# Kernel optimization log

Hardware: AMD Instinct MI355X
Metric: run time of the kernel (lower is better)

Reference implementation:

```python
import jax, jax.numpy as jnp
import numpy as np

D = 512  # c_size == q_size


def setup_inputs() -> dict:
    key = jax.random.key(0)
    ks = jax.random.split(key, 8)
    c = jax.random.normal(ks[0], (8, 2048, D), dtype=jnp.float32)
    q = jax.random.normal(ks[1], (8, 512, D), dtype=jnp.float32)
    sc = 1.0 / np.sqrt(D)
    w_c = jax.random.uniform(ks[2], (D,), jnp.float32, -sc, sc)
    b_c = jax.random.uniform(ks[3], (), jnp.float32, -sc, sc)
    w_q = jax.random.uniform(ks[4], (D,), jnp.float32, -sc, sc)
    b_q = jax.random.uniform(ks[5], (), jnp.float32, -sc, sc)
    w_cq = jax.random.uniform(ks[6], (D,), jnp.float32, -sc, sc)
    b_cq = jax.random.uniform(ks[7], (), jnp.float32, -sc, sc)
    return {"c": c, "q": q, "w_c": w_c, "b_c": b_c, "w_q": w_q, "b_q": b_q,
            "w_cq": w_cq, "b_cq": b_cq}


def reference(c, q, w_c, b_c, w_q, b_q, w_cq, b_cq):
    # s[b,t,i] = <c[b,t],w_c>+b_c + <q[b,i],w_q>+b_q + <c[b,t]*q[b,i], w_cq>+b_cq
    # The original per-query-token loop for att_weight_cq(c*qi) collapses to
    # a single batched contraction since the Linear is linear in c*qi.
    sc = jnp.einsum('btd,d->bt', c, w_c) + b_c          # (B, c_len)
    sq = jnp.einsum('bid,d->bi', q, w_q) + b_q          # (B, q_len)
    scq = jnp.einsum('btd,bid->bti', c * w_cq, q) + b_cq  # (B, c_len, q_len)
    s = sc[:, :, None] + sq[:, None, :] + scq

    a = jax.nn.softmax(s, axis=2)                       # attend over q
    c2q = jnp.einsum('bti,bid->btd', a, q)              # (B, c_len, D)

    b = jax.nn.softmax(jnp.max(s, axis=2), axis=1)      # (B, c_len)
    q2c = jnp.einsum('bt,btd->bd', b, c)                # (B, D)
    q2c = jnp.broadcast_to(q2c[:, None, :], c.shape)    # (B, c_len, D)

    x = jnp.concatenate([c, c2q, c * c2q, c * q2c], axis=-1)
    return x
```

## Files before the change

kernel.cpp:

```cpp
#include <hip/hip_runtime.h>
#include <cstdint>


constexpr int kB = 8;
constexpr int kT = 2048;
constexpr int kI = 512;
constexpr int kD = 512;
constexpr int kW = 4 * kD;
constexpr int kRows = 64;
constexpr int kTiles = kT / kRows;
constexpr int kChunk = kRows * 72;

using f32x4  = __attribute__((ext_vector_type(4))) float;
using bf16x4 = __attribute__((ext_vector_type(4))) __bf16;
using bf16x8 = __attribute__((ext_vector_type(8))) __bf16;

__device__ __forceinline__ float dot8(const f32x4& a0, const f32x4& a1,
                                      const f32x4& b0, const f32x4& b1) {
  return a0.x * b0.x + a0.y * b0.y + a0.z * b0.z + a0.w * b0.w +
         a1.x * b1.x + a1.y * b1.y + a1.z * b1.z + a1.w * b1.w;
}

__global__ __launch_bounds__(256) void prep_kernel(
    const float* __restrict__ q, const float* __restrict__ w_q,
    const float* __restrict__ b_q, float* __restrict__ sq,
    __bf16* __restrict__ qf, __bf16* __restrict__ vf) {
  const int b = blockIdx.y;
  const int tid = threadIdx.x;
  if (blockIdx.x < 32) {
    __shared__ float sacc[16][17];
    const int g = blockIdx.x;
    const int kk0 = tid >> 6;
    const int lane = tid & 63;
    const int lr = lane & 15, lg = lane >> 4;
    const float* row = q + ((size_t)(b * kI + g * 16 + lr)) * kD;
    float sp = 0.f;
#pragma unroll
    for (int kk = kk0; kk < 16; kk += 4) {
      const int ka = kk * 32 + lg * 8;
      f32x4 v0 = *(const f32x4*)(row + ka);
      f32x4 v1 = *(const f32x4*)(row + ka + 4);
      f32x4 u0 = *(const f32x4*)(w_q + ka);
      f32x4 u1 = *(const f32x4*)(w_q + ka + 4);
      sp += dot8(v0, v1, u0, u1);
      bf16x8 o = {(__bf16)v0.x, (__bf16)v0.y, (__bf16)v0.z, (__bf16)v0.w,
                  (__bf16)v1.x, (__bf16)v1.y, (__bf16)v1.z, (__bf16)v1.w};
      *(bf16x8*)(qf + ((((size_t)(b * 32 + g)) * 16 + kk) << 9) + lane * 8) = o;
    }
    sacc[lr][kk0 * 4 + lg] = sp;
    __syncthreads();
    if (tid < 16) {
      float s = 0.f;
#pragma unroll
      for (int j = 0; j < 16; ++j) s += sacc[tid][j];
      sq[b * kI + g * 16 + tid] = s + b_q[0];
    }
  } else {
    __shared__ float ts[64][68];
    const int blk = blockIdx.x - 32;
    const int i0 = (blk & 7) * 64;
    const int d0 = (blk >> 3) * 64;
    const int r = tid >> 2;
    const int cg = (tid & 3) * 16;
#pragma unroll
    for (int j = 0; j < 4; ++j) {
      f32x4 v = *(const f32x4*)(q + ((size_t)(b * kI + i0 + r)) * kD + d0 + cg + 4 * j);
      ts[r][cg + 4 * j + 0] = v.x;
      ts[r][cg + 4 * j + 1] = v.y;
      ts[r][cg + 4 * j + 2] = v.z;
      ts[r][cg + 4 * j + 3] = v.w;
    }
    __syncthreads();
    const int dl = tid >> 2;
    const int ig = (tid & 3) * 16;
    bf16x8 o0, o1;
#pragma unroll
    for (int j = 0; j < 8; ++j) o0[j] = (__bf16)ts[ig + j][dl];
#pragma unroll
    for (int j = 0; j < 8; ++j) o1[j] = (__bf16)ts[ig + 8 + j][dl];
    const int gd = (d0 >> 4) + (dl >> 4);
    const int lr = dl & 15;
    const int kki0 = (i0 >> 5) + (ig >> 5);
    const int lg0 = (ig & 31) >> 3;
    const int i1 = ig + 8;
    const int kki1 = (i0 >> 5) + (i1 >> 5);
    const int lg1 = (i1 & 31) >> 3;
    *(bf16x8*)(vf + ((((size_t)(b * 32 + gd)) * 16 + kki0) << 9) +
               (lg0 * 16 + lr) * 8) = o0;
    *(bf16x8*)(vf + ((((size_t)(b * 32 + gd)) * 16 + kki1) << 9) +
               (lg1 * 16 + lr) * 8) = o1;
  }
}

__global__ __launch_bounds__(512, 1) void fused_attn(
    const float* __restrict__ c, const __bf16* __restrict__ qf,
    const __bf16* __restrict__ vf, const float* __restrict__ w_cq,
    const float* __restrict__ w_c, const float* __restrict__ b_c,
    const float* __restrict__ b_cq, const float* __restrict__ sq,
    float* __restrict__ out, float* __restrict__ mz,
    float* __restrict__ u_tile) {
  __shared__ __align__(16) char lAP[16 * kChunk];
  __shared__ float scrow[kRows];
  __shared__ float redm[8 * kRows];
  __shared__ float reds[8 * kRows];

  const int b = blockIdx.y;
  const int tile = blockIdx.x;
  const int t0 = tile * kRows;
  const int tid = threadIdx.x;
  const int w = tid >> 6;
  const int lane = tid & 63;
  const int lr = lane & 15, lg = lane >> 4;

  const __bf16* qfb = qf + (((size_t)(b * 32 + w * 4)) * 16 << 9) + lane * 8;
  bf16x8 b0[4], b1[4], b2[4], b3[4];
#pragma unroll
  for (int n4 = 0; n4 < 4; ++n4)
    b0[n4] = *(const bf16x8*)(qfb + (((size_t)(n4 * 16 + 0)) << 9));
#pragma unroll
  for (int n4 = 0; n4 < 4; ++n4)
    b1[n4] = *(const bf16x8*)(qfb + (((size_t)(n4 * 16 + 1)) << 9));
#pragma unroll
  for (int n4 = 0; n4 < 4; ++n4)
    b2[n4] = *(const bf16x8*)(qfb + (((size_t)(n4 * 16 + 2)) << 9));

  {
    const int srow = tid >> 3;
    const int col4 = (tid & 7) * 4;
    const float* crow = c + ((size_t)(b * kT + t0 + srow)) * kD;
    float* orow0 = out + ((size_t)(b * kT + t0 + srow)) * kW;
    float scp = 0.f;
#pragma unroll
    for (int j = 0; j < 16; ++j) {
      const int col = col4 + j * 32;
      f32x4 v = *(const f32x4*)(crow + col);
      *(f32x4*)(orow0 + col) = v;
      const f32x4 wq = *(const f32x4*)(w_cq + col);
      const f32x4 wc = *(const f32x4*)(w_c + col);
      scp += v.x * wc.x + v.y * wc.y + v.z * wc.z + v.w * wc.w;
      v *= wq;
      bf16x4 bv = {(__bf16)v.x, (__bf16)v.y, (__bf16)v.z, (__bf16)v.w};
      *(bf16x4*)(lAP + j * kChunk + srow * 72 + col4 * 2) = bv;
    }
    scp += __shfl_xor(scp, 1, 64);
    scp += __shfl_xor(scp, 2, 64);
    scp += __shfl_xor(scp, 4, 64);
    if ((tid & 7) == 0) scrow[srow] = scp + b_c[0];
  }
  __syncthreads();

  f32x4 acc[4][4] = {};
  bf16x8 afc[4], afn[4];
#pragma unroll
  for (int m = 0; m < 4; ++m)
    afc[m] = *(const bf16x8*)(lAP + 0 * kChunk + (m * 16 + lr) * 72 + lg * 16);
#pragma unroll
  for (int kk = 0; kk < 16; ++kk) {
    if (kk < 13) {
#pragma unroll
      for (int n4 = 0; n4 < 4; ++n4)
        b3[n4] = *(const bf16x8*)(qfb + (((size_t)(n4 * 16 + kk + 3)) << 9));
    }
    if (kk < 15) {
#pragma unroll
      for (int m = 0; m < 4; ++m)
        afn[m] = *(const bf16x8*)(lAP + (kk + 1) * kChunk + (m * 16 + lr) * 72 +
                                  lg * 16);
    }
#pragma unroll
    for (int m = 0; m < 4; ++m)
#pragma unroll
      for (int n4 = 0; n4 < 4; ++n4)
        acc[m][n4] = __builtin_amdgcn_mfma_f32_16x16x32_bf16(afc[m], b0[n4],
                                                             acc[m][n4], 0, 0, 0);
#pragma unroll
    for (int m = 0; m < 4; ++m) afc[m] = afn[m];
#pragma unroll
    for (int n4 = 0; n4 < 4; ++n4) {
      b0[n4] = b1[n4];
      b1[n4] = b2[n4];
      b2[n4] = b3[n4];
    }
  }

  const float bq = b_cq[0];
  float sqv[4];
#pragma unroll
  for (int n4 = 0; n4 < 4; ++n4) sqv[n4] = sq[b * kI + w * 64 + n4 * 16 + lr];
  float scr[4][4];
#pragma unroll
  for (int m = 0; m < 4; ++m)
#pragma unroll
    for (int r = 0; r < 4; ++r) scr[m][r] = scrow[m * 16 + lg * 4 + r] + bq;
#pragma unroll
  for (int m = 0; m < 4; ++m)
#pragma unroll
    for (int n4 = 0; n4 < 4; ++n4)
#pragma unroll
      for (int r = 0; r < 4; ++r) acc[m][n4][r] += scr[m][r] + sqv[n4];

  float mx[4][4];
#pragma unroll
  for (int m = 0; m < 4; ++m)
#pragma unroll
    for (int r = 0; r < 4; ++r) {
      float v = acc[m][0][r];
#pragma unroll
      for (int n4 = 1; n4 < 4; ++n4) v = fmaxf(v, acc[m][n4][r]);
#pragma unroll
      for (int off = 1; off <= 8; off <<= 1) v = fmaxf(v, __shfl_xor(v, off, 64));
      mx[m][r] = v;
    }
  if (lr == 0) {
#pragma unroll
    for (int m = 0; m < 4; ++m)
#pragma unroll
      for (int r = 0; r < 4; ++r)
        redm[w * kRows + m * 16 + lg * 4 + r] = mx[m][r];
  }
  __syncthreads();
#pragma unroll
  for (int m = 0; m < 4; ++m)
#pragma unroll
    for (int r = 0; r < 4; ++r) {
      const int rw = m * 16 + lg * 4 + r;
      float v = redm[rw];
#pragma unroll
      for (int w2 = 1; w2 < 8; ++w2) v = fmaxf(v, redm[w2 * kRows + rw]);
      mx[m][r] = v;
    }

  float sm[4][4] = {};
#pragma unroll
  for (int m = 0; m < 4; ++m)
#pragma unroll
    for (int n4 = 0; n4 < 4; ++n4)
#pragma unroll
      for (int r = 0; r < 4; ++r) {
        const float p = __expf(acc[m][n4][r] - mx[m][r]);
        acc[m][n4][r] = p;
        sm[m][r] += p;
      }
#pragma unroll
  for (int m = 0; m < 4; ++m)
#pragma unroll
    for (int r = 0; r < 4; ++r)
#pragma unroll
      for (int off = 1; off <= 8; off <<= 1)
        sm[m][r] += __shfl_xor(sm[m][r], off, 64);
  if (lr == 0) {
#pragma unroll
    for (int m = 0; m < 4; ++m)
#pragma unroll
      for (int r = 0; r < 4; ++r)
        reds[w * kRows + m * 16 + lg * 4 + r] = sm[m][r];
  }
  __syncthreads();
  float inv[4][4];
#pragma unroll
  for (int m = 0; m < 4; ++m)
#pragma unroll
    for (int r = 0; r < 4; ++r) {
      const int rw = m * 16 + lg * 4 + r;
      float v = reds[rw];
#pragma unroll
      for (int w2 = 1; w2 < 8; ++w2) v += reds[w2 * kRows + rw];
      inv[m][r] = 1.f / v;
    }

  const __bf16* vfb = vf + (((size_t)(b * 32 + w * 4)) * 16 << 9) + lane * 8;
  bf16x8 v0_[4], v1_[4], v2_[4], v3_[4];
#pragma unroll
  for (int n4 = 0; n4 < 4; ++n4)
    v0_[n4] = *(const bf16x8*)(vfb + (((size_t)(n4 * 16 + 0)) << 9));
#pragma unroll
  for (int n4 = 0; n4 < 4; ++n4)
    v1_[n4] = *(const bf16x8*)(vfb + (((size_t)(n4 * 16 + 1)) << 9));
#pragma unroll
  for (int n4 = 0; n4 < 4; ++n4)
    v2_[n4] = *(const bf16x8*)(vfb + (((size_t)(n4 * 16 + 2)) << 9));

#pragma unroll
  for (int m = 0; m < 4; ++m)
#pragma unroll
    for (int r = 0; r < 4; ++r) {
      const int trow = m * 16 + lg * 4 + r;
#pragma unroll
      for (int n4 = 0; n4 < 4; ++n4) {
        const int icol = w * 64 + n4 * 16 + lr;
        const int kkc = icol >> 5, kc = icol & 31;
        *(__bf16*)(lAP + kkc * kChunk + trow * 72 + kc * 2) =
            (__bf16)(acc[m][n4][r] * inv[m][r]);
      }
    }
  __syncthreads();

  float cfrag[4][4][4];
#pragma unroll
  for (int m = 0; m < 4; ++m)
#pragma unroll
    for (int r = 0; r < 4; ++r) {
      const float* crow2 =
          c + ((size_t)(b * kT + t0 + m * 16 + lg * 4 + r)) * kD + w * 64 + lr;
#pragma unroll
      for (int n4 = 0; n4 < 4; ++n4) cfrag[m][n4][r] = crow2[n4 * 16];
    }

  f32x4 o[4][4] = {};
  bf16x8 pfc[4], pfn[4];
#pragma unroll
  for (int m = 0; m < 4; ++m)
    pfc[m] = *(const bf16x8*)(lAP + 0 * kChunk + (m * 16 + lr) * 72 + lg * 16);
#pragma unroll
  for (int kki = 0; kki < 16; ++kki) {
    if (kki < 13) {
#pragma unroll
      for (int n4 = 0; n4 < 4; ++n4)
        v3_[n4] = *(const bf16x8*)(vfb + (((size_t)(n4 * 16 + kki + 3)) << 9));
    }
    if (kki < 15) {
#pragma unroll
      for (int m = 0; m < 4; ++m)
        pfn[m] = *(const bf16x8*)(lAP + (kki + 1) * kChunk + (m * 16 + lr) * 72 +
                                  lg * 16);
    }
#pragma unroll
    for (int m = 0; m < 4; ++m)
#pragma unroll
      for (int n4 = 0; n4 < 4; ++n4)
        o[m][n4] = __builtin_amdgcn_mfma_f32_16x16x32_bf16(pfc[m], v0_[n4],
                                                           o[m][n4], 0, 0, 0);
#pragma unroll
    for (int m = 0; m < 4; ++m) pfc[m] = pfn[m];
#pragma unroll
    for (int n4 = 0; n4 < 4; ++n4) {
      v0_[n4] = v1_[n4];
      v1_[n4] = v2_[n4];
      v2_[n4] = v3_[n4];
    }
  }

  float m_tile;
  {
    float v = mx[0][0];
#pragma unroll
    for (int m = 0; m < 4; ++m)
#pragma unroll
      for (int r = 0; r < 4; ++r) v = fmaxf(v, mx[m][r]);
    v = fmaxf(v, __shfl_xor(v, 16, 64));
    v = fmaxf(v, __shfl_xor(v, 32, 64));
    m_tile = v;
  }
  float u[4] = {};
  float zz = 0.f;
#pragma unroll
  for (int m = 0; m < 4; ++m)
#pragma unroll
    for (int r = 0; r < 4; ++r) {
      const int t = t0 + m * 16 + lg * 4 + r;
      const size_t rb = (size_t)(b * kT + t);
      float* orow = out + rb * kW;
      const float ev = __expf(mx[m][r] - m_tile);
      zz += ev;
#pragma unroll
      for (int n4 = 0; n4 < 4; ++n4) {
        const int d = w * 64 + n4 * 16 + lr;
        const float cvv = cfrag[m][n4][r];
        const float pv = o[m][n4][r];
        orow[kD + d] = pv;
        orow[2 * kD + d] = cvv * pv;
        u[n4] += ev * cvv;
      }
    }
#pragma unroll
  for (int n4 = 0; n4 < 4; ++n4) {
    u[n4] += __shfl_xor(u[n4], 16, 64);
    u[n4] += __shfl_xor(u[n4], 32, 64);
  }
  if (lg == 0) {
    float* ub = u_tile + ((size_t)(b * kTiles + tile)) * kD;
#pragma unroll
    for (int n4 = 0; n4 < 4; ++n4) ub[w * 64 + n4 * 16 + lr] = u[n4];
  }
  if (w == 0) {
    zz += __shfl_xor(zz, 16, 64);
    zz += __shfl_xor(zz, 32, 64);
    if (lane == 0) {
      mz[b * 64 + tile] = m_tile;
      mz[b * 64 + 32 + tile] = zz;
    }
  }
}

__global__ __launch_bounds__(512) void slot3_merge_kernel(
    const float* __restrict__ mz, const float* __restrict__ u_tile,
    float* __restrict__ out) {
  const int b = blockIdx.y;
  const int tile = blockIdx.x;
  const int t0 = tile * kRows;
  const int tid = threadIdx.x;
  __shared__ float sM[32], sZ[32];
  __shared__ float sq2c[kD];
  if (tid < 32) {
    sM[tid] = mz[b * 64 + tid];
    sZ[tid] = mz[b * 64 + 32 + tid];
  }
  __syncthreads();
  {
    float M = sM[0];
#pragma unroll
    for (int k = 1; k < 32; ++k) M = fmaxf(M, sM[k]);
    float Z = 0.f;
    float s = 0.f;
#pragma unroll
    for (int k = 0; k < 32; ++k) {
      const float wk = __expf(sM[k] - M);
      Z += wk * sZ[k];
      s += wk * u_tile[((size_t)(b * kTiles + k)) * kD + tid];
    }
    sq2c[tid] = s / Z;
  }
  __syncthreads();
  const int srow = tid >> 3;
  const int col4 = (tid & 7) * 4;
  const size_t rb = (size_t)(b * kT + t0 + srow);
  float* orow = out + rb * kW;
#pragma unroll
  for (int j = 0; j < 16; ++j) {
    const int col = col4 + j * 32;
    const f32x4 cv = *(const f32x4*)(orow + col);
    const f32x4 qc = *(const f32x4*)(sq2c + col);
    *(f32x4*)(orow + 3 * kD + col) = cv * qc;
  }
}

extern "C" void kernel_launch(void* const* d_in, const int* in_sizes, int n_in,
                              void* d_out, int out_size, void* d_ws, size_t ws_size,
                              hipStream_t stream) {
  const float* c    = (const float*)d_in[0];
  const float* q    = (const float*)d_in[1];
  const float* w_c  = (const float*)d_in[2];
  const float* b_c  = (const float*)d_in[3];
  const float* w_q  = (const float*)d_in[4];
  const float* b_q  = (const float*)d_in[5];
  const float* w_cq = (const float*)d_in[6];
  const float* b_cq = (const float*)d_in[7];
  float* out = (float*)d_out;
  float* ws = (float*)d_ws;

  float* sq     = ws;
  float* mz     = sq + kB * kI;
  float* u_tile = mz + kB * 64;
  __bf16* qf = (__bf16*)(u_tile + (size_t)kB * kTiles * kD);
  __bf16* vf = qf + (size_t)kB * kI * kD;

  dim3 gp(96, kB);
  prep_kernel<<<gp, 256, 0, stream>>>(q, w_q, b_q, sq, qf, vf);

  dim3 gf(kTiles, kB);
  fused_attn<<<gf, 512, 0, stream>>>(c, qf, vf, w_cq, w_c, b_c, b_cq, sq, out,
                                     mz, u_tile);

  slot3_merge_kernel<<<gf, 512, 0, stream>>>(mz, u_tile, out);
}
```

Baseline: 68.07 us.

## Fuse q2c merge into attention kernel via per-batch atomic grid barrier

```diff
diff --git a/kernel.cpp b/kernel.cpp
--- a/kernel.cpp
+++ b/kernel.cpp
@@ -24,9 +24,10 @@
 __global__ __launch_bounds__(256) void prep_kernel(
     const float* __restrict__ q, const float* __restrict__ w_q,
     const float* __restrict__ b_q, float* __restrict__ sq,
-    __bf16* __restrict__ qf, __bf16* __restrict__ vf) {
+    __bf16* __restrict__ qf, __bf16* __restrict__ vf, int* __restrict__ ctr) {
   const int b = blockIdx.y;
   const int tid = threadIdx.x;
+  if (blockIdx.x == 0 && tid == 0) ctr[b] = 0;
   if (blockIdx.x < 32) {
     __shared__ float sacc[16][17];
     const int g = blockIdx.x;
@@ -98,11 +99,12 @@
     const float* __restrict__ w_c, const float* __restrict__ b_c,
     const float* __restrict__ b_cq, const float* __restrict__ sq,
     float* __restrict__ out, float* __restrict__ mz,
-    float* __restrict__ u_tile) {
+    float* __restrict__ u_tile, int* __restrict__ ctr) {
   __shared__ __align__(16) char lAP[16 * kChunk];
   __shared__ float scrow[kRows];
   __shared__ float redm[8 * kRows];
   __shared__ float reds[8 * kRows];
+  __shared__ float sq2c[kD];
 
   const int b = blockIdx.y;
   const int tile = blockIdx.x;
@@ -390,48 +392,48 @@
       mz[b * 64 + 32 + tile] = zz;
     }
   }
-}
-
-__global__ __launch_bounds__(512) void slot3_merge_kernel(
-    const float* __restrict__ mz, const float* __restrict__ u_tile,
-    float* __restrict__ out) {
-  const int b = blockIdx.y;
-  const int tile = blockIdx.x;
-  const int t0 = tile * kRows;
-  const int tid = threadIdx.x;
-  __shared__ float sM[32], sZ[32];
-  __shared__ float sq2c[kD];
-  if (tid < 32) {
-    sM[tid] = mz[b * 64 + tid];
-    sZ[tid] = mz[b * 64 + 32 + tid];
-  }
+
+  __threadfence();
+  __syncthreads();
+  if (tid == 0) {
+    __hip_atomic_fetch_add(&ctr[b], 1, __ATOMIC_ACQ_REL,
+                           __HIP_MEMORY_SCOPE_AGENT);
+    while (__hip_atomic_load(&ctr[b], __ATOMIC_ACQUIRE,
+                             __HIP_MEMORY_SCOPE_AGENT) < kTiles) {
+    }
+  }
+  __syncthreads();
+
+  if (tid < 64) redm[tid] = mz[b * 64 + tid];
   __syncthreads();
   {
-    float M = sM[0];
-#pragma unroll
-    for (int k = 1; k < 32; ++k) M = fmaxf(M, sM[k]);
+    float M = redm[0];
+#pragma unroll
+    for (int k = 1; k < 32; ++k) M = fmaxf(M, redm[k]);
     float Z = 0.f;
     float s = 0.f;
 #pragma unroll
     for (int k = 0; k < 32; ++k) {
-      const float wk = __expf(sM[k] - M);
-      Z += wk * sZ[k];
+      const float wk = __expf(redm[k] - M);
+      Z += wk * redm[32 + k];
       s += wk * u_tile[((size_t)(b * kTiles + k)) * kD + tid];
     }
     sq2c[tid] = s / Z;
   }
   __syncthreads();
-  const int srow = tid >> 3;
-  const int col4 = (tid & 7) * 4;
-  const size_t rb = (size_t)(b * kT + t0 + srow);
-  float* orow = out + rb * kW;
-#pragma unroll
-  for (int j = 0; j < 16; ++j) {
-    const int col = col4 + j * 32;
-    const f32x4 cv = *(const f32x4*)(orow + col);
-    const f32x4 qc = *(const f32x4*)(sq2c + col);
-    *(f32x4*)(orow + 3 * kD + col) = cv * qc;
-  }
+
+#pragma unroll
+  for (int m = 0; m < 4; ++m)
+#pragma unroll
+    for (int r = 0; r < 4; ++r) {
+      const int t = t0 + m * 16 + lg * 4 + r;
+      float* orow3 = out + ((size_t)(b * kT + t)) * kW + 3 * kD;
+#pragma unroll
+      for (int n4 = 0; n4 < 4; ++n4) {
+        const int d = w * 64 + n4 * 16 + lr;
+        orow3[d] = cfrag[m][n4][r] * sq2c[d];
+      }
+    }
 }
 
 extern "C" void kernel_launch(void* const* d_in, const int* in_sizes, int n_in,
@@ -451,15 +453,14 @@
   float* sq     = ws;
   float* mz     = sq + kB * kI;
   float* u_tile = mz + kB * 64;
-  __bf16* qf = (__bf16*)(u_tile + (size_t)kB * kTiles * kD);
+  int*   ctr    = (int*)(u_tile + (size_t)kB * kTiles * kD);
+  __bf16* qf = (__bf16*)(ctr + 8);
   __bf16* vf = qf + (size_t)kB * kI * kD;
 
   dim3 gp(96, kB);
-  prep_kernel<<<gp, 256, 0, stream>>>(q, w_q, b_q, sq, qf, vf);
+  prep_kernel<<<gp, 256, 0, stream>>>(q, w_q, b_q, sq, qf, vf, ctr);
 
   dim3 gf(kTiles, kB);
   fused_attn<<<gf, 512, 0, stream>>>(c, qf, vf, w_cq, w_c, b_c, b_cq, sq, out,
-                                     mz, u_tile);
-
-  slot3_merge_kernel<<<gf, 512, 0, stream>>>(mz, u_tile, out);
+                                     mz, u_tile, ctr);
 }
```

New measurement: 156.9 us. +130.5%, slower.
